# Kernel tuning notes

Hardware: AMD Instinct MI355X
Metric: run time of the kernel (lower is better)

The kernel has to match this reference:

```python
import jax, jax.numpy as jnp
import numpy as np


def _chamfer_single_directional(x, y):
    """Mean over batch of mean over points of min_j ||x_i - y_j||^2.

    x: [B, N, 3] (predicted), y: [B, M, 3] (target).
    Matches pytorch3d chamfer_distance(x, y, single_directional=True)
    with norm=2, point_reduction='mean', batch_reduction='mean'.
    """
    x2 = jnp.sum(x * x, axis=-1)                      # [B, N]
    y2 = jnp.sum(y * y, axis=-1)                      # [B, M]
    cross = jnp.einsum('bnd,bmd->bnm', x, y)          # [B, N, M]
    d2 = x2[:, :, None] + y2[:, None, :] - 2.0 * cross  # squared L2
    min_d2 = jnp.min(d2, axis=2)                      # [B, N] nearest in y
    return jnp.mean(jnp.mean(min_d2, axis=1))         # scalar


def setup_inputs() -> dict:
    key = jax.random.key(0)
    k1, k2 = jax.random.split(key)
    v = jax.random.normal(k1, (4, 8192, 3), dtype=jnp.float32)
    v_pred = jax.random.normal(k2, (4, 8192, 3), dtype=jnp.float32)
    return {"v": v, "v_pred": v_pred}


def reference(v, v_pred):
    # forward: chamfer_distance(v_pred, v, single_directional=True)
    return _chamfer_single_directional(v_pred, v)
```

## Files before the change

### kernel.cpp

```cpp
#include <hip/hip_runtime.h>

#define BB 4
#define NN 8192
#define MM 8192
#define BN (BB * NN)

#define BLK 256
#define QB  256
#define TC  1024
#define S   (MM / TC)
#define NJT (TC / 32)
#define NGRP ((NN / QB) * BB)

#define RB 32
#define GPB (NGRP / RB)

typedef __bf16 bf16x8 __attribute__((ext_vector_type(8)));
typedef float  f32x16 __attribute__((ext_vector_type(16)));


static __device__ inline void split_bf(float v, __bf16& h, __bf16& l) {
    h = (__bf16)v;
    l = (__bf16)(v - (float)h);
}

__global__ __launch_bounds__(BLK, 4) void chamfer_part(
    const float* __restrict__ y,
    const float* __restrict__ x,
    float* __restrict__ part)
{
    __shared__ uint4 FR[NJT * 64];
    __shared__ float red[QB];

    const int t   = threadIdx.x;
    const int l   = t & 63;
    const int w   = t >> 6;
    const int hi  = l >> 5;
    const int c32 = l & 31;
    const int ib  = blockIdx.x;
    const int s   = blockIdx.y;
    const int b   = blockIdx.z;
    const int g   = b * (NN / QB) + ib;

    {
        const float* xb = x + ((size_t)b * NN + (size_t)ib * QB) * 3;
        float x0 = xb[3*t+0], x1 = xb[3*t+1], x2 = xb[3*t+2];
        __bf16 h0,l0,h1,l1,h2,l2;
        split_bf(2.0f*x0, h0, l0);
        split_bf(2.0f*x1, h1, l1);
        split_bf(2.0f*x2, h2, l2);
        float nxx = -__builtin_fmaf(x2, x2, __builtin_fmaf(x1, x1, x0*x0));
        __bf16 hx, lx; split_bf(nxx, hx, lx);
        const __bf16 one = (__bf16)1.0f;
        bf16x8 g0 = {h0,h0,l0,l0,h1,h1,l1,l1};
        bf16x8 g1 = {h2,h2,l2,l2,hx,lx,one,one};
        const int at = t >> 5, col = t & 31;
        FR[at*64 +      col] = __builtin_bit_cast(uint4, g0);
        FR[at*64 + 32 + col] = __builtin_bit_cast(uint4, g1);
    }
    __syncthreads();
    const bf16x8 a0 = __builtin_bit_cast(bf16x8, FR[(w*2 + 0)*64 + l]);
    const bf16x8 a1 = __builtin_bit_cast(bf16x8, FR[(w*2 + 1)*64 + l]);
    __syncthreads();

    {
        const float* yb = y + ((size_t)b * MM + (size_t)s * TC) * 3;
        const __bf16 one = (__bf16)1.0f;
#pragma unroll
        for (int k2 = 0; k2 < 4; ++k2) {
            const int j = t + k2 * BLK;
            float y0 = yb[3*j+0], y1 = yb[3*j+1], y2 = yb[3*j+2];
            __bf16 h0,l0,h1,l1,h2,l2;
            split_bf(y0, h0, l0);
            split_bf(y1, h1, l1);
            split_bf(y2, h2, l2);
            float nyy = -__builtin_fmaf(y2, y2, __builtin_fmaf(y1, y1, y0*y0));
            __bf16 hy, ly; split_bf(nyy, hy, ly);
            bf16x8 g0 = {h0,l0,h0,l0,h1,l1,h1,l1};
            bf16x8 g1 = {h2,l2,h2,l2,one,one,hy,ly};
            const int jt = j >> 5, col = j & 31;
            FR[jt*64 +      col] = __builtin_bit_cast(uint4, g0);
            FR[jt*64 + 32 + col] = __builtin_bit_cast(uint4, g1);
        }
    }
    __syncthreads();

    f32x16 z;
#pragma unroll
    for (int r = 0; r < 16; ++r) z[r] = 0.0f;
    f32x16 best0, best1;
#pragma unroll
    for (int r = 0; r < 16; ++r) { best0[r] = -3.4e38f; best1[r] = -3.4e38f; }

#pragma unroll 1
    for (int jt = 0; jt < NJT; jt += 2) {
        const bf16x8 bf0 = __builtin_bit_cast(bf16x8, FR[jt*64 + l]);
        const bf16x8 bf1 = __builtin_bit_cast(bf16x8, FR[jt*64 + 64 + l]);
        f32x16 p = __builtin_amdgcn_mfma_f32_32x32x16_bf16(a0, bf0, z, 0, 0, 0);
        f32x16 q = __builtin_amdgcn_mfma_f32_32x32x16_bf16(a0, bf1, z, 0, 0, 0);
#pragma unroll
        for (int r = 0; r < 16; ++r)
            best0[r] = fmaxf(fmaxf(best0[r], p[r]), q[r]);
        p = __builtin_amdgcn_mfma_f32_32x32x16_bf16(a1, bf0, z, 0, 0, 0);
        q = __builtin_amdgcn_mfma_f32_32x32x16_bf16(a1, bf1, z, 0, 0, 0);
#pragma unroll
        for (int r = 0; r < 16; ++r)
            best1[r] = fmaxf(fmaxf(best1[r], p[r]), q[r]);
    }

#pragma unroll
    for (int ii = 0; ii < 2; ++ii) {
        const f32x16 bb = ii ? best1 : best0;
#pragma unroll
        for (int r = 0; r < 16; ++r) {
            float v = bb[r];
            v = fmaxf(v, __shfl_xor(v, 1, 64));
            v = fmaxf(v, __shfl_xor(v, 2, 64));
            v = fmaxf(v, __shfl_xor(v, 4, 64));
            v = fmaxf(v, __shfl_xor(v, 8, 64));
            v = fmaxf(v, __shfl_xor(v, 16, 64));
            if (c32 == 0) {
                const int qrow = (w*2 + ii)*32 + (r & 3) + 8*(r >> 2) + 4*hi;
                red[qrow] = -v;
            }
        }
    }
    __syncthreads();
    part[((size_t)g * S + s) * QB + t] = red[t];
}

__global__ __launch_bounds__(BLK) void reduce_groups(
    const float* __restrict__ part,
    float* __restrict__ ws2)
{
    const int t = threadIdx.x;
    float acc = 0.0f;
#pragma unroll
    for (int gi = 0; gi < GPB; ++gi) {
        const float* pg = part + ((size_t)(blockIdx.x * GPB + gi) * S) * QB;
        float dq = pg[t];
#pragma unroll
        for (int ss = 1; ss < S; ++ss)
            dq = fminf(dq, pg[ss * QB + t]);
        acc += dq;
    }
    for (int off = 32; off > 0; off >>= 1)
        acc += __shfl_down(acc, off, 64);
    __shared__ float wsum[4];
    if ((t & 63) == 0) wsum[t >> 6] = acc;
    __syncthreads();
    if (t == 0)
        ws2[blockIdx.x] = wsum[0] + wsum[1] + wsum[2] + wsum[3];
}

__global__ __launch_bounds__(64) void final32(
    const float* __restrict__ ws2,
    float* __restrict__ out)
{
    const int t = threadIdx.x;
    float v = (t < RB) ? ws2[t] : 0.0f;
    for (int off = 32; off > 0; off >>= 1)
        v += __shfl_down(v, off, 64);
    if (t == 0) out[0] = v * (1.0f / (float)BN);
}

extern "C" void kernel_launch(void* const* d_in, const int* in_sizes, int n_in,
                              void* d_out, int out_size, void* d_ws, size_t ws_size,
                              hipStream_t stream) {
    const float* v      = (const float*)d_in[0];
    const float* v_pred = (const float*)d_in[1];
    float* out = (float*)d_out;

    float* part = (float*)d_ws;
    float* ws2  = (float*)((char*)d_ws + (1u << 20));

    chamfer_part<<<dim3(NN / QB, S, BB), BLK, 0, stream>>>(v, v_pred, part);
    reduce_groups<<<RB, BLK, 0, stream>>>(part, ws2);
    final32<<<1, 64, 0, stream>>>(ws2, out);
}
```

Baseline: 73.44 us.

## Shuffle-build A fragments, prefetch B fragments, merge reductions into one kernel

The A-operand fragments are now built with wave shuffles instead of an LDS round trip, which removes two block barriers. The main loop double-buffers its LDS reads of B fragments two tile-pairs ahead so the loads overlap the MFMAs. The two reduction kernels are replaced by a single 1024-thread block to save a kernel launch, at the cost of serialising the min-reduction through one block.

```diff
diff --git a/kernel.cpp b/kernel.cpp
--- a/kernel.cpp
+++ b/kernel.cpp
@@ -11,9 +11,6 @@
 #define S   (MM / TC)
 #define NJT (TC / 32)
 #define NGRP ((NN / QB) * BB)
-
-#define RB 32
-#define GPB (NGRP / RB)
 
 typedef __bf16 bf16x8 __attribute__((ext_vector_type(8)));
 typedef float  f32x16 __attribute__((ext_vector_type(16)));
@@ -42,6 +39,7 @@
     const int b   = blockIdx.z;
     const int g   = b * (NN / QB) + ib;
 
+    bf16x8 a0, a1;
     {
         const float* xb = x + ((size_t)b * NN + (size_t)ib * QB) * 3;
         float x0 = xb[3*t+0], x1 = xb[3*t+1], x2 = xb[3*t+2];
@@ -54,14 +52,26 @@
         const __bf16 one = (__bf16)1.0f;
         bf16x8 g0 = {h0,h0,l0,l0,h1,h1,l1,l1};
         bf16x8 g1 = {h2,h2,l2,l2,hx,lx,one,one};
-        const int at = t >> 5, col = t & 31;
-        FR[at*64 +      col] = __builtin_bit_cast(uint4, g0);
-        FR[at*64 + 32 + col] = __builtin_bit_cast(uint4, g1);
+        uint4 u0 = __builtin_bit_cast(uint4, g0);
+        uint4 u1 = __builtin_bit_cast(uint4, g1);
+
+        int p0x = __shfl((int)u0.x, c32, 64), p1x = __shfl((int)u1.x, c32, 64);
+        int p0y = __shfl((int)u0.y, c32, 64), p1y = __shfl((int)u1.y, c32, 64);
+        int p0z = __shfl((int)u0.z, c32, 64), p1z = __shfl((int)u1.z, c32, 64);
+        int p0w = __shfl((int)u0.w, c32, 64), p1w = __shfl((int)u1.w, c32, 64);
+        int q0x = __shfl((int)u0.x, 32+c32, 64), q1x = __shfl((int)u1.x, 32+c32, 64);
+        int q0y = __shfl((int)u0.y, 32+c32, 64), q1y = __shfl((int)u1.y, 32+c32, 64);
+        int q0z = __shfl((int)u0.z, 32+c32, 64), q1z = __shfl((int)u1.z, 32+c32, 64);
+        int q0w = __shfl((int)u0.w, 32+c32, 64), q1w = __shfl((int)u1.w, 32+c32, 64);
+
+        uint4 r0, r1;
+        r0.x = (unsigned)(hi ? p1x : p0x);  r0.y = (unsigned)(hi ? p1y : p0y);
+        r0.z = (unsigned)(hi ? p1z : p0z);  r0.w = (unsigned)(hi ? p1w : p0w);
+        r1.x = (unsigned)(hi ? q1x : q0x);  r1.y = (unsigned)(hi ? q1y : q0y);
+        r1.z = (unsigned)(hi ? q1z : q0z);  r1.w = (unsigned)(hi ? q1w : q0w);
+        a0 = __builtin_bit_cast(bf16x8, r0);
+        a1 = __builtin_bit_cast(bf16x8, r1);
     }
-    __syncthreads();
-    const bf16x8 a0 = __builtin_bit_cast(bf16x8, FR[(w*2 + 0)*64 + l]);
-    const bf16x8 a1 = __builtin_bit_cast(bf16x8, FR[(w*2 + 1)*64 + l]);
-    __syncthreads();
 
     {
         const float* yb = y + ((size_t)b * MM + (size_t)s * TC) * 3;
@@ -92,20 +102,26 @@
 #pragma unroll
     for (int r = 0; r < 16; ++r) { best0[r] = -3.4e38f; best1[r] = -3.4e38f; }
 
+    bf16x8 c0 = __builtin_bit_cast(bf16x8, FR[0*64 + l]);
+    bf16x8 c1 = __builtin_bit_cast(bf16x8, FR[1*64 + l]);
+    bf16x8 n0 = __builtin_bit_cast(bf16x8, FR[2*64 + l]);
+    bf16x8 n1 = __builtin_bit_cast(bf16x8, FR[3*64 + l]);
+
 #pragma unroll 1
     for (int jt = 0; jt < NJT; jt += 2) {
-        const bf16x8 bf0 = __builtin_bit_cast(bf16x8, FR[jt*64 + l]);
-        const bf16x8 bf1 = __builtin_bit_cast(bf16x8, FR[jt*64 + 64 + l]);
-        f32x16 p = __builtin_amdgcn_mfma_f32_32x32x16_bf16(a0, bf0, z, 0, 0, 0);
-        f32x16 q = __builtin_amdgcn_mfma_f32_32x32x16_bf16(a0, bf1, z, 0, 0, 0);
+        bf16x8 f0 = __builtin_bit_cast(bf16x8, FR[((jt+4) & 31)*64 + l]);
+        bf16x8 f1 = __builtin_bit_cast(bf16x8, FR[((jt+5) & 31)*64 + l]);
+        f32x16 p = __builtin_amdgcn_mfma_f32_32x32x16_bf16(a0, c0, z, 0, 0, 0);
+        f32x16 q = __builtin_amdgcn_mfma_f32_32x32x16_bf16(a0, c1, z, 0, 0, 0);
 #pragma unroll
         for (int r = 0; r < 16; ++r)
             best0[r] = fmaxf(fmaxf(best0[r], p[r]), q[r]);
-        p = __builtin_amdgcn_mfma_f32_32x32x16_bf16(a1, bf0, z, 0, 0, 0);
-        q = __builtin_amdgcn_mfma_f32_32x32x16_bf16(a1, bf1, z, 0, 0, 0);
+        p = __builtin_amdgcn_mfma_f32_32x32x16_bf16(a1, c0, z, 0, 0, 0);
+        q = __builtin_amdgcn_mfma_f32_32x32x16_bf16(a1, c1, z, 0, 0, 0);
 #pragma unroll
         for (int r = 0; r < 16; ++r)
             best1[r] = fmaxf(fmaxf(best1[r], p[r]), q[r]);
+        c0 = n0; c1 = n1; n0 = f0; n1 = f1;
     }
 
 #pragma unroll
@@ -129,39 +145,34 @@
     part[((size_t)g * S + s) * QB + t] = red[t];
 }
 
-__global__ __launch_bounds__(BLK) void reduce_groups(
+__global__ __launch_bounds__(1024) void reduce_one(
     const float* __restrict__ part,
-    float* __restrict__ ws2)
+    float* __restrict__ out)
 {
     const int t = threadIdx.x;
+    const int q = t & 255;
     float acc = 0.0f;
-#pragma unroll
-    for (int gi = 0; gi < GPB; ++gi) {
-        const float* pg = part + ((size_t)(blockIdx.x * GPB + gi) * S) * QB;
-        float dq = pg[t];
+#pragma unroll 2
+    for (int i = 0; i < NGRP / 4; ++i) {
+        const int gidx = (t >> 8) + 4 * i;
+        const float* pg = part + (size_t)gidx * S * QB + q;
+        float dq = pg[0];
 #pragma unroll
         for (int ss = 1; ss < S; ++ss)
-            dq = fminf(dq, pg[ss * QB + t]);
+            dq = fminf(dq, pg[ss * QB]);
         acc += dq;
     }
     for (int off = 32; off > 0; off >>= 1)
         acc += __shfl_down(acc, off, 64);
-    __shared__ float wsum[4];
+    __shared__ float wsum[16];
     if ((t & 63) == 0) wsum[t >> 6] = acc;
     __syncthreads();
-    if (t == 0)
-        ws2[blockIdx.x] = wsum[0] + wsum[1] + wsum[2] + wsum[3];
-}
-
-__global__ __launch_bounds__(64) void final32(
-    const float* __restrict__ ws2,
-    float* __restrict__ out)
-{
-    const int t = threadIdx.x;
-    float v = (t < RB) ? ws2[t] : 0.0f;
-    for (int off = 32; off > 0; off >>= 1)
-        v += __shfl_down(v, off, 64);
-    if (t == 0) out[0] = v * (1.0f / (float)BN);
+    if (t == 0) {
+        float tot = 0.0f;
+#pragma unroll
+        for (int i = 0; i < 16; ++i) tot += wsum[i];
+        out[0] = tot * (1.0f / (float)BN);
+    }
 }
 
 extern "C" void kernel_launch(void* const* d_in, const int* in_sizes, int n_in,
@@ -172,9 +183,7 @@
     float* out = (float*)d_out;
 
     float* part = (float*)d_ws;
-    float* ws2  = (float*)((char*)d_ws + (1u << 20));
 
     chamfer_part<<<dim3(NN / QB, S, BB), BLK, 0, stream>>>(v, v_pred, part);
-    reduce_groups<<<RB, BLK, 0, stream>>>(part, ws2);
-    final32<<<1, 64, 0, stream>>>(ws2, out);
+    reduce_one<<<1, 1024, 0, stream>>>(part, out);
 }
```

New measurement: 82.79 us. +12.7%, slower.
